# Kernel optimization log

Measured on AMD Instinct MI355X. Metric: run time of the kernel, lower is better.

## Reference

```python
import jax, jax.numpy as jnp
import numpy as np


def setup_inputs() -> dict:
    key = jax.random.key(0)
    ks = jax.random.split(key, 7)
    B, H, W, C = 8, 64, 64, 8
    d = C // 8  # q/k/v channels (= 1 here; forced by the module's broadcast-add)
    x = jax.random.normal(ks[0], (B, H, W, C), dtype=jnp.float32)
    # 1x1 convs == per-pixel linear layers: weight (C, d), bias (d,)
    scale = 1.0 / np.sqrt(C)
    Wq = jax.random.normal(ks[1], (C, d), dtype=jnp.float32) * scale
    bq = jnp.zeros((d,), dtype=jnp.float32)
    Wk = jax.random.normal(ks[2], (C, d), dtype=jnp.float32) * scale
    bk = jnp.zeros((d,), dtype=jnp.float32)
    Wv = jax.random.normal(ks[3], (C, d), dtype=jnp.float32) * scale
    bv = jnp.zeros((d,), dtype=jnp.float32)
    gamma = jnp.float32(0.5)  # nonzero so the attention branch matters
    return {"x": x, "Wq": Wq, "bq": bq, "Wk": Wk, "bk": bk, "Wv": Wv, "bv": bv, "gamma": gamma}


def reference(x, Wq, bq, Wk, bk, Wv, bv, gamma):
    B, H, W, C = x.shape
    N = H * W
    # 1x1 conv projections (NHWC, per-pixel linear)
    q = (jnp.einsum('bhwc,cd->bhwd', x, Wq) + bq).reshape(B, N, -1)  # (B,N,d)
    k = (jnp.einsum('bhwc,cd->bhwd', x, Wk) + bk).reshape(B, N, -1)  # (B,N,d)
    v = (jnp.einsum('bhwc,cd->bhwd', x, Wv) + bv).reshape(B, N, -1)  # (B,N,d)
    # energy[b,i,j] = <q_i, k_j>; NOTE: no 1/sqrt(d) scaling, per source
    energy = jnp.einsum('bnd,bmd->bnm', q, k)  # (B,N,N)
    attention = jax.nn.softmax(energy, axis=-1)
    # out[b,i,d] = sum_j attention[b,i,j] * v[b,j,d]
    out = jnp.einsum('bnm,bmd->bnd', attention, v).reshape(B, H, W, -1)  # (B,H,W,d)
    # gamma-scaled residual; d==1 so out broadcasts against C channels
    y = out * gamma + x
    return (y, attention)
```

## Files before the change

### kernel.cpp

```cpp
#include <hip/hip_runtime.h>
#include <math.h>

#define NPIX 4096
#define CCH 8
#define ROWS 64
#define BLK 256
#define NW   (BLK/64)
#define L2E 1.44269504088896340736f

typedef float floatx4 __attribute__((ext_vector_type(4)));

__global__ __launch_bounds__(BLK) void attn_fused(
    const float* __restrict__ x,
    const float* __restrict__ Wq, const float* __restrict__ bq,
    const float* __restrict__ Wk, const float* __restrict__ bk,
    const float* __restrict__ Wv, const float* __restrict__ bv,
    const float* __restrict__ gamma_p,
    float* __restrict__ y, float* __restrict__ attn)
{
    __shared__ float ks[NPIX];
    __shared__ float vs[NPIX];
    __shared__ float qrow[ROWS];
    __shared__ float crow[ROWS];
    __shared__ float spart[NW][ROWS];
    __shared__ float opart[NW][ROWS];
    __shared__ float kred[2][NW];

    const int b = blockIdx.y;
    const int rowbase = blockIdx.x * ROWS;
    const int tid = threadIdx.x;
    const int wid = tid >> 6;
    const int lane = tid & 63;

    float wq[CCH], wk[CCH], wv[CCH];
#pragma unroll
    for (int c = 0; c < CCH; ++c) { wq[c] = Wq[c]; wk[c] = Wk[c]; wv[c] = Wv[c]; }
    const float bqv = bq[0], bkv = bk[0], bvv = bv[0];
    const float gamma = gamma_p[0];

    const float* xb = x + (size_t)b * NPIX * CCH;

    float kmx = -INFINITY, kmn = INFINITY;
    for (int j = tid; j < NPIX; j += BLK) {
        const float4* xp = reinterpret_cast<const float4*>(xb + (size_t)j * CCH);
        float4 x0 = xp[0];
        float4 x1 = xp[1];
        float kj = bkv;
        kj = fmaf(x0.x, wk[0], kj); kj = fmaf(x0.y, wk[1], kj);
        kj = fmaf(x0.z, wk[2], kj); kj = fmaf(x0.w, wk[3], kj);
        kj = fmaf(x1.x, wk[4], kj); kj = fmaf(x1.y, wk[5], kj);
        kj = fmaf(x1.z, wk[6], kj); kj = fmaf(x1.w, wk[7], kj);
        float vj = bvv;
        vj = fmaf(x0.x, wv[0], vj); vj = fmaf(x0.y, wv[1], vj);
        vj = fmaf(x0.z, wv[2], vj); vj = fmaf(x0.w, wv[3], vj);
        vj = fmaf(x1.x, wv[4], vj); vj = fmaf(x1.y, wv[5], vj);
        vj = fmaf(x1.z, wv[6], vj); vj = fmaf(x1.w, wv[7], vj);
        ks[j] = kj;
        vs[j] = vj;
        kmx = fmaxf(kmx, kj);
        kmn = fminf(kmn, kj);
    }
#pragma unroll
    for (int off = 32; off > 0; off >>= 1) {
        kmx = fmaxf(kmx, __shfl_xor(kmx, off));
        kmn = fminf(kmn, __shfl_xor(kmn, off));
    }
    if (lane == 0) { kred[0][wid] = kmx; kred[1][wid] = kmn; }
    __syncthreads();
    kmx = fmaxf(fmaxf(kred[0][0], kred[0][1]), fmaxf(kred[0][2], kred[0][3]));
    kmn = fminf(fminf(kred[1][0], kred[1][1]), fminf(kred[1][2], kred[1][3]));

    const int r = lane;
    const int i = rowbase + r;
    const float4* xq = reinterpret_cast<const float4*>(xb + (size_t)i * CCH);
    float4 a0 = xq[0];
    float4 a1 = xq[1];
    float q = bqv;
    q = fmaf(a0.x, wq[0], q); q = fmaf(a0.y, wq[1], q);
    q = fmaf(a0.z, wq[2], q); q = fmaf(a0.w, wq[3], q);
    q = fmaf(a1.x, wq[4], q); q = fmaf(a1.y, wq[5], q);
    q = fmaf(a1.z, wq[6], q); q = fmaf(a1.w, wq[7], q);

    const float q2 = q * L2E;
    const float m2 = q2 * ((q >= 0.f) ? kmx : kmn);

    float s0 = 0.f, s1 = 0.f, s2 = 0.f, s3 = 0.f;
    float o0 = 0.f, o1 = 0.f, o2 = 0.f, o3 = 0.f;
    const int j0 = wid * (NPIX / NW);
    for (int j = j0; j < j0 + NPIX / NW; j += 4) {
        float4 kk = *reinterpret_cast<const float4*>(&ks[j]);
        float4 vv = *reinterpret_cast<const float4*>(&vs[j]);
        float e0 = exp2f(fmaf(q2, kk.x, -m2));
        float e1 = exp2f(fmaf(q2, kk.y, -m2));
        float e2 = exp2f(fmaf(q2, kk.z, -m2));
        float e3 = exp2f(fmaf(q2, kk.w, -m2));
        s0 += e0; s1 += e1; s2 += e2; s3 += e3;
        o0 = fmaf(e0, vv.x, o0);
        o1 = fmaf(e1, vv.y, o1);
        o2 = fmaf(e2, vv.z, o2);
        o3 = fmaf(e3, vv.w, o3);
    }
    spart[wid][r] = (s0 + s1) + (s2 + s3);
    opart[wid][r] = (o0 + o1) + (o2 + o3);
    __syncthreads();

    if (tid < ROWS) {
        const float s = (spart[0][tid] + spart[1][tid]) + (spart[2][tid] + spart[3][tid]);
        const float o = (opart[0][tid] + opart[1][tid]) + (opart[2][tid] + opart[3][tid]);
        const float outv = o / s;
        const float og = outv * gamma;
        const int i2 = rowbase + tid;
        const float4* xr = reinterpret_cast<const float4*>(xb + (size_t)i2 * CCH);
        float4 b0 = xr[0];
        float4 b1 = xr[1];
        float* yp = y + ((size_t)b * NPIX + i2) * CCH;
        float4 y0 = { og + b0.x, og + b0.y, og + b0.z, og + b0.w };
        float4 y1 = { og + b1.x, og + b1.y, og + b1.z, og + b1.w };
        *reinterpret_cast<float4*>(yp) = y0;
        *reinterpret_cast<float4*>(yp + 4) = y1;
        qrow[tid] = q2;
        crow[tid] = m2 + log2f(s);
    }
    __syncthreads();

    float* ap0 = attn + ((size_t)b * NPIX + rowbase) * (size_t)NPIX;
    for (int rr = 0; rr < ROWS; ++rr) {
        const float qr = qrow[rr];
        const float cr = crow[rr];
        float* ap = ap0 + (size_t)rr * NPIX;
#pragma unroll
        for (int j4 = tid * 4; j4 < NPIX; j4 += BLK * 4) {
            float4 kk = *reinterpret_cast<const float4*>(&ks[j4]);
            floatx4 e;
            e.x = exp2f(fmaf(qr, kk.x, -cr));
            e.y = exp2f(fmaf(qr, kk.y, -cr));
            e.z = exp2f(fmaf(qr, kk.z, -cr));
            e.w = exp2f(fmaf(qr, kk.w, -cr));
            __builtin_nontemporal_store(e, reinterpret_cast<floatx4*>(&ap[j4]));
        }
    }
}

extern "C" void kernel_launch(void* const* d_in, const int* in_sizes, int n_in,
                              void* d_out, int out_size, void* d_ws, size_t ws_size,
                              hipStream_t stream) {
    const float* x   = (const float*)d_in[0];
    const float* Wq  = (const float*)d_in[1];
    const float* bq  = (const float*)d_in[2];
    const float* Wk  = (const float*)d_in[3];
    const float* bk  = (const float*)d_in[4];
    const float* Wv  = (const float*)d_in[5];
    const float* bv  = (const float*)d_in[6];
    const float* gm  = (const float*)d_in[7];

    const int B = in_sizes[0] / (NPIX * CCH);
    float* y    = (float*)d_out;
    float* attn = y + (size_t)B * NPIX * CCH;

    dim3 grid(NPIX / ROWS, B);
    attn_fused<<<grid, BLK, 0, stream>>>(x, Wq, bq, Wk, bk, Wv, bv, gm, y, attn);
}
```

Before: 136.2 us.

## Split rows across all threads with per-row wave reductions and register-cached keys

Halves the rows per block so the grid has twice as many blocks. The row-statistics pass is restructured so every thread holds its slice of k/v in registers, loops over all rows, and reduces sums with wave shuffles, instead of one lane per row scanning a quarter of the keys. The attention write loop reuses the register-cached keys rather than re-reading LDS, and it switches from nontemporal stores to plain stores. The cost is that each block now recomputes the full k/v projection for only 32 rows, which doubles that redundant work, and there are 32 shuffle reductions per block.

```diff
diff --git a/kernel.cpp b/kernel.cpp
--- a/kernel.cpp
+++ b/kernel.cpp
@@ -3,7 +3,7 @@
 
 #define NPIX 4096
 #define CCH 8
-#define ROWS 64
+#define ROWS 32
 #define BLK 256
 #define NW   (BLK/64)
 #define L2E 1.44269504088896340736f
@@ -21,6 +21,7 @@
     __shared__ float ks[NPIX];
     __shared__ float vs[NPIX];
     __shared__ float qrow[ROWS];
+    __shared__ float mrow[ROWS];
     __shared__ float crow[ROWS];
     __shared__ float spart[NW][ROWS];
     __shared__ float opart[NW][ROWS];
@@ -70,73 +71,84 @@
     kmx = fmaxf(fmaxf(kred[0][0], kred[0][1]), fmaxf(kred[0][2], kred[0][3]));
     kmn = fminf(fminf(kred[1][0], kred[1][1]), fminf(kred[1][2], kred[1][3]));
 
-    const int r = lane;
-    const int i = rowbase + r;
-    const float4* xq = reinterpret_cast<const float4*>(xb + (size_t)i * CCH);
-    float4 a0 = xq[0];
-    float4 a1 = xq[1];
-    float q = bqv;
-    q = fmaf(a0.x, wq[0], q); q = fmaf(a0.y, wq[1], q);
-    q = fmaf(a0.z, wq[2], q); q = fmaf(a0.w, wq[3], q);
-    q = fmaf(a1.x, wq[4], q); q = fmaf(a1.y, wq[5], q);
-    q = fmaf(a1.z, wq[6], q); q = fmaf(a1.w, wq[7], q);
+    const int j4 = tid * 4;
+    float4 kc[4], vc[4];
+#pragma unroll
+    for (int g = 0; g < 4; ++g) {
+        kc[g] = *reinterpret_cast<const float4*>(&ks[j4 + g * 1024]);
+        vc[g] = *reinterpret_cast<const float4*>(&vs[j4 + g * 1024]);
+    }
 
-    const float q2 = q * L2E;
-    const float m2 = q2 * ((q >= 0.f) ? kmx : kmn);
+    if (tid < ROWS) {
+        const int i = rowbase + tid;
+        const float4* xq = reinterpret_cast<const float4*>(xb + (size_t)i * CCH);
+        float4 a0 = xq[0];
+        float4 a1 = xq[1];
+        float q = bqv;
+        q = fmaf(a0.x, wq[0], q); q = fmaf(a0.y, wq[1], q);
+        q = fmaf(a0.z, wq[2], q); q = fmaf(a0.w, wq[3], q);
+        q = fmaf(a1.x, wq[4], q); q = fmaf(a1.y, wq[5], q);
+        q = fmaf(a1.z, wq[6], q); q = fmaf(a1.w, wq[7], q);
+        const float q2 = q * L2E;
+        qrow[tid] = q2;
+        mrow[tid] = q2 * ((q >= 0.f) ? kmx : kmn);
+    }
+    __syncthreads();
 
-    float s0 = 0.f, s1 = 0.f, s2 = 0.f, s3 = 0.f;
-    float o0 = 0.f, o1 = 0.f, o2 = 0.f, o3 = 0.f;
-    const int j0 = wid * (NPIX / NW);
-    for (int j = j0; j < j0 + NPIX / NW; j += 4) {
-        float4 kk = *reinterpret_cast<const float4*>(&ks[j]);
-        float4 vv = *reinterpret_cast<const float4*>(&vs[j]);
-        float e0 = exp2f(fmaf(q2, kk.x, -m2));
-        float e1 = exp2f(fmaf(q2, kk.y, -m2));
-        float e2 = exp2f(fmaf(q2, kk.z, -m2));
-        float e3 = exp2f(fmaf(q2, kk.w, -m2));
-        s0 += e0; s1 += e1; s2 += e2; s3 += e3;
-        o0 = fmaf(e0, vv.x, o0);
-        o1 = fmaf(e1, vv.y, o1);
-        o2 = fmaf(e2, vv.z, o2);
-        o3 = fmaf(e3, vv.w, o3);
+    for (int rr = 0; rr < ROWS; ++rr) {
+        const float q2r = qrow[rr];
+        const float m2r = mrow[rr];
+        float s = 0.f, o = 0.f;
+#pragma unroll
+        for (int g = 0; g < 4; ++g) {
+            float e0 = exp2f(fmaf(q2r, kc[g].x, -m2r));
+            float e1 = exp2f(fmaf(q2r, kc[g].y, -m2r));
+            float e2 = exp2f(fmaf(q2r, kc[g].z, -m2r));
+            float e3 = exp2f(fmaf(q2r, kc[g].w, -m2r));
+            s += (e0 + e1) + (e2 + e3);
+            float t0 = fmaf(e0, vc[g].x, e1 * vc[g].y);
+            float t1 = fmaf(e2, vc[g].z, e3 * vc[g].w);
+            o += t0 + t1;
+        }
+#pragma unroll
+        for (int off = 32; off > 0; off >>= 1) {
+            s += __shfl_xor(s, off);
+            o += __shfl_xor(o, off);
+        }
+        if (lane == 0) { spart[wid][rr] = s; opart[wid][rr] = o; }
     }
-    spart[wid][r] = (s0 + s1) + (s2 + s3);
-    opart[wid][r] = (o0 + o1) + (o2 + o3);
     __syncthreads();
 
     if (tid < ROWS) {
         const float s = (spart[0][tid] + spart[1][tid]) + (spart[2][tid] + spart[3][tid]);
         const float o = (opart[0][tid] + opart[1][tid]) + (opart[2][tid] + opart[3][tid]);
-        const float outv = o / s;
-        const float og = outv * gamma;
-        const int i2 = rowbase + tid;
-        const float4* xr = reinterpret_cast<const float4*>(xb + (size_t)i2 * CCH);
+        const float og = (o / s) * gamma;
+        const int i = rowbase + tid;
+        const float4* xr = reinterpret_cast<const float4*>(xb + (size_t)i * CCH);
         float4 b0 = xr[0];
         float4 b1 = xr[1];
-        float* yp = y + ((size_t)b * NPIX + i2) * CCH;
+        float* yp = y + ((size_t)b * NPIX + i) * CCH;
         float4 y0 = { og + b0.x, og + b0.y, og + b0.z, og + b0.w };
         float4 y1 = { og + b1.x, og + b1.y, og + b1.z, og + b1.w };
         *reinterpret_cast<float4*>(yp) = y0;
         *reinterpret_cast<float4*>(yp + 4) = y1;
-        qrow[tid] = q2;
-        crow[tid] = m2 + log2f(s);
+        crow[tid] = mrow[tid] + log2f(s);
     }
     __syncthreads();
 
-    float* ap0 = attn + ((size_t)b * NPIX + rowbase) * (size_t)NPIX;
+    float* ap0 = attn + ((size_t)b * NPIX + rowbase) * (size_t)NPIX + j4;
     for (int rr = 0; rr < ROWS; ++rr) {
         const float qr = qrow[rr];
         const float cr = crow[rr];
         float* ap = ap0 + (size_t)rr * NPIX;
 #pragma unroll
-        for (int j4 = tid * 4; j4 < NPIX; j4 += BLK * 4) {
-            float4 kk = *reinterpret_cast<const float4*>(&ks[j4]);
-            floatx4 e;
-            e.x = exp2f(fmaf(qr, kk.x, -cr));
-            e.y = exp2f(fmaf(qr, kk.y, -cr));
-            e.z = exp2f(fmaf(qr, kk.z, -cr));
-            e.w = exp2f(fmaf(qr, kk.w, -cr));
-            __builtin_nontemporal_store(e, reinterpret_cast<floatx4*>(&ap[j4]));
+        for (int g = 0; g < 4; ++g) {
+            float4 e;
+            e.x = exp2f(fmaf(qr, kc[g].x, -cr));
+            e.y = exp2f(fmaf(qr, kc[g].y, -cr));
+            e.z = exp2f(fmaf(qr, kc[g].z, -cr));
+            e.w = exp2f(fmaf(qr, kc[g].w, -cr));
+            *reinterpret_cast<float4*>(ap + g * 1024) = e;
         }
     }
 }
```

New measurement: 131.5 us. -3.5%, faster.
